# Kernel tuning notes

Measured on AMD Instinct MI355X. Metric: run time of the kernel, lower is better.

Reference implementation:

```python
import jax, jax.numpy as jnp
import numpy as np

N_NODES = 100000
N_EDGES = 1600000
IN_F = 64
HID_F = 64
HID_CH = 32
OUT_F = 16


def setup_inputs() -> dict:
    key = jax.random.key(0)
    ks = jax.random.split(key, 12)
    feat = jax.random.normal(ks[0], (N_NODES, IN_F), dtype=jnp.float32)
    edge_src = jax.random.randint(ks[1], (N_EDGES,), 0, N_NODES, dtype=jnp.int32)
    edge_dst = jax.random.randint(ks[2], (N_EDGES,), 0, N_NODES, dtype=jnp.int32)
    s = 1.414 / np.sqrt(IN_F)
    fc1_w = jax.random.normal(ks[3], (HID_F, IN_F), dtype=jnp.float32) * s
    fc1_b = jnp.zeros((HID_F,), dtype=jnp.float32)
    filt_w = jax.random.normal(ks[4], (HID_F, IN_F), dtype=jnp.float32) * s
    filt_b = jnp.zeros((HID_F,), dtype=jnp.float32)
    att_w1 = jax.random.normal(ks[5], (HID_F, HID_CH), dtype=jnp.float32) * (1.0 / np.sqrt(HID_F))
    att_b1 = jnp.zeros((HID_CH,), dtype=jnp.float32)
    att_w2 = jax.random.normal(ks[6], (HID_CH, 1), dtype=jnp.float32) * (1.0 / np.sqrt(HID_CH))
    fc2_w = jax.random.normal(ks[7], (OUT_F, HID_F), dtype=jnp.float32) * (1.414 / np.sqrt(HID_F))
    fc2_b = jnp.zeros((OUT_F,), dtype=jnp.float32)
    return {
        "feat": feat, "edge_src": edge_src, "edge_dst": edge_dst,
        "fc1_w": fc1_w, "fc1_b": fc1_b, "filt_w": filt_w, "filt_b": filt_b,
        "att_w1": att_w1, "att_b1": att_b1, "att_w2": att_w2,
        "fc2_w": fc2_w, "fc2_b": fc2_b,
    }


def _lp_filter(feat, edge_src, edge_dst, filt_w, filt_b):
    # Low-pass (GCN-style) filter: symmetric-normalized neighborhood aggregation
    # of the linearly transformed features.  x: [N, H]
    x = feat @ filt_w.T + filt_b
    ones = jnp.ones((edge_src.shape[0],), dtype=x.dtype)
    deg_out = jax.ops.segment_sum(ones, edge_src, num_segments=N_NODES)
    deg_in = jax.ops.segment_sum(ones, edge_dst, num_segments=N_NODES)
    inv_sqrt_out = jax.lax.rsqrt(jnp.maximum(deg_out, 1.0))
    inv_sqrt_in = jax.lax.rsqrt(jnp.maximum(deg_in, 1.0))
    # gather-transform-scatter: msg_e = x[src_e] * norm_e  ->  sum at dst
    coef = inv_sqrt_out[edge_src] * inv_sqrt_in[edge_dst]  # [E]
    msg = x[edge_src] * coef[:, None]                       # [E, H]
    return jax.ops.segment_sum(msg, edge_dst, num_segments=N_NODES)  # [N, H]


def _channel_attention(z, att_w1, att_b1, att_w2):
    # z: [N, C, H]; semantic (channel) attention a la HAN
    w = jnp.tanh(z @ att_w1 + att_b1) @ att_w2        # [N, C, 1]
    beta = jax.nn.softmax(w.mean(axis=0), axis=0)     # [C, 1]
    return (beta[None, :, :] * z).sum(axis=1)         # [N, H]


def reference(feat, edge_src, edge_dst, fc1_w, fc1_b, filt_w, filt_b,
              att_w1, att_b1, att_w2, fc2_w, fc2_b):
    h1 = jnp.tanh(feat @ fc1_w.T + fc1_b)                          # MLP branch [N, H]
    h2 = _lp_filter(feat, edge_src, edge_dst, filt_w, filt_b)      # graph branch [N, H]
    z = jnp.stack([h1, h2], axis=1)                                # [N, 2, H]
    fused = _channel_attention(z, att_w1, att_b1, att_w2)          # [N, H]
    return fused @ fc2_w.T + fc2_b                                 # [N, OUT_F]
```

## Files before the change

### kernel.cpp

```cpp
#include <hip/hip_runtime.h>
#include <math.h>

#define N_NODESC 100000
#define N_EDGESC 1600000
#define NBUCK 1563
#define BSLACK 1280
#define SCHUNK 4096
#define NSBLK 391

__device__ __forceinline__ float fast_tanh(float x) {
    float ax = fabsf(x);
    float e = __expf(-2.f * ax);
    float r = (1.f - e) * __builtin_amdgcn_rcpf(1.f + e);
    return copysignf(r, x);
}

__global__ void binit_kernel(int* __restrict__ bcur, int* __restrict__ sbcur) {
    int i = blockIdx.x * blockDim.x + threadIdx.x;
    if (i < NBUCK) { bcur[i] = i * BSLACK; sbcur[i] = i * BSLACK; }
}

__global__ __launch_bounds__(1024) void scatter_dual_kernel(
    const int* __restrict__ src, const int* __restrict__ dst,
    int* __restrict__ bcur, int* __restrict__ sbcur,
    unsigned* __restrict__ bedges, unsigned char* __restrict__ sbytes) {
    __shared__ int histd[NBUCK];
    __shared__ int hists[NBUCK];
    int tid = threadIdx.x;
    int e_beg = blockIdx.x * SCHUNK;
    int e_end = min(e_beg + SCHUNK, N_EDGESC);
    for (int i = tid; i < NBUCK; i += 1024) { histd[i] = 0; hists[i] = 0; }
    __syncthreads();

    int ss[4], dd[4];
    int cnt = 0;
    for (int i = e_beg + tid; i < e_end; i += 1024) {
        ss[cnt] = src[i];
        dd[cnt] = dst[i];
        cnt++;
    }
#pragma unroll
    for (int j = 0; j < 4; j++) {
        if (j < cnt) {
            atomicAdd(&histd[dd[j] >> 6], 1);
            atomicAdd(&hists[ss[j] >> 6], 1);
        }
    }
    __syncthreads();
    for (int i = tid; i < NBUCK; i += 1024) {
        int c = histd[i];
        if (c > 0) histd[i] = atomicAdd(&bcur[i], c);
        int c2 = hists[i];
        if (c2 > 0) hists[i] = atomicAdd(&sbcur[i], c2);
    }
    __syncthreads();
#pragma unroll
    for (int j = 0; j < 4; j++) {
        if (j < cnt) {
            int slot = atomicAdd(&histd[dd[j] >> 6], 1);
            bedges[slot] = (unsigned)ss[j] | ((unsigned)(dd[j] & 63) << 17);
            int slot2 = atomicAdd(&hists[ss[j] >> 6], 1);
            sbytes[slot2] = (unsigned char)(ss[j] & 63);
        }
    }
}

__global__ __launch_bounds__(256) void gemm_kernel(
    const float* __restrict__ feat,
    const float* __restrict__ w1, const float* __restrict__ b1,
    const float* __restrict__ w2, const float* __restrict__ b2,
    const int* __restrict__ sbcur, const unsigned char* __restrict__ sbytes,
    float* __restrict__ h1, float* __restrict__ xs) {
    __shared__ float sf[128 * 68];
    __shared__ int ldeg[128];
    int tid = threadIdx.x;
    int base = blockIdx.x * 128;
    if (tid < 128) ldeg[tid] = 0;
    for (int k = 0; k < 8; k++) {
        int fi = tid + k * 256;
        int node = fi >> 4, f4 = fi & 15;
        float4 v = make_float4(0.f, 0.f, 0.f, 0.f);
        if (base + node < N_NODESC)
            v = ((const float4*)feat)[(size_t)(base + node) * 16 + f4];
        float* d = &sf[node * 68 + f4 * 4];
        d[0] = v.x; d[1] = v.y; d[2] = v.z; d[3] = v.w;
    }
    __syncthreads();

#pragma unroll
    for (int h = 0; h < 2; h++) {
        int sb = blockIdx.x * 2 + h;
        if (sb < NBUCK) {
            int sbeg = sb * BSLACK;
            int sm = sbcur[sb] - sbeg;
            for (int i = tid; i < sm; i += 256)
                atomicAdd(&ldeg[h * 64 + (int)sbytes[sbeg + i]], 1);
        }
    }

    int lane = tid & 63;
    int og = __builtin_amdgcn_readfirstlane(tid >> 6);
    const float* wp1 = w1 + og * 16 * 64;
    const float* wp2 = w2 + og * 16 * 64;

    float a1[2][16], a2[2][16];
#pragma unroll
    for (int o = 0; o < 16; o++) {
        float bb1 = b1[og * 16 + o], bb2 = b2[og * 16 + o];
        a1[0][o] = bb1; a1[1][o] = bb1;
        a2[0][o] = bb2; a2[1][o] = bb2;
    }

    for (int fq = 0; fq < 16; fq++) {
        float4 fv0 = *(const float4*)&sf[lane * 68 + fq * 4];
        float4 fv1 = *(const float4*)&sf[(lane + 64) * 68 + fq * 4];
#pragma unroll
        for (int o = 0; o < 16; o++) {
            float4 wv1 = *(const float4*)&wp1[o * 64 + fq * 4];
            float4 wv2 = *(const float4*)&wp2[o * 64 + fq * 4];
            a1[0][o] += fv0.x * wv1.x + fv0.y * wv1.y + fv0.z * wv1.z + fv0.w * wv1.w;
            a1[1][o] += fv1.x * wv1.x + fv1.y * wv1.y + fv1.z * wv1.z + fv1.w * wv1.w;
            a2[0][o] += fv0.x * wv2.x + fv0.y * wv2.y + fv0.z * wv2.z + fv0.w * wv2.w;
            a2[1][o] += fv1.x * wv2.x + fv1.y * wv2.y + fv1.z * wv2.z + fv1.w * wv2.w;
        }
    }

    __syncthreads();

#pragma unroll
    for (int j = 0; j < 2; j++) {
        int g = base + lane + j * 64;
        if (g >= N_NODESC) continue;
        float is = rsqrtf(fmaxf((float)ldeg[j * 64 + lane], 1.f));
#pragma unroll
        for (int oq = 0; oq < 4; oq++) {
            float4 t, u;
            t.x = fast_tanh(a1[j][oq * 4 + 0]); t.y = fast_tanh(a1[j][oq * 4 + 1]);
            t.z = fast_tanh(a1[j][oq * 4 + 2]); t.w = fast_tanh(a1[j][oq * 4 + 3]);
            u.x = a2[j][oq * 4 + 0] * is;   u.y = a2[j][oq * 4 + 1] * is;
            u.z = a2[j][oq * 4 + 2] * is;   u.w = a2[j][oq * 4 + 3] * is;
            ((float4*)h1)[(size_t)g * 16 + og * 4 + oq] = t;
            ((float4*)xs)[(size_t)g * 16 + og * 4 + oq] = u;
        }
    }
}

__global__ __launch_bounds__(256) void agg4_kernel(const int* __restrict__ bcur,
                                                   const unsigned* __restrict__ bedges,
                                                   const float* __restrict__ xs,
                                                   float* __restrict__ h2) {
    __shared__ unsigned eraw[BSLACK];
    __shared__ unsigned eled[BSLACK];
    __shared__ int loff[65];
    __shared__ int lcnt[64];
    __shared__ int lcur[64];
    int tid = threadIdx.x, lane = tid & 63, wid = tid >> 6;
    int b = blockIdx.x;
    int beg = b * BSLACK;
    int m = bcur[b] - beg;

    if (tid < 64) lcnt[tid] = 0;
    __syncthreads();
    for (int i = tid; i < m; i += 256) {
        unsigned pk = bedges[beg + i];
        eraw[i] = pk;
        atomicAdd(&lcnt[pk >> 17], 1);
    }
    __syncthreads();
    if (wid == 0) {
        int c = lcnt[lane];
        int v = c;
#pragma unroll
        for (int off = 1; off < 64; off <<= 1) {
            int t = __shfl_up(v, off, 64);
            if (lane >= off) v += t;
        }
        loff[lane] = v - c;
        lcur[lane] = v - c;
        if (lane == 63) loff[64] = v;
    }
    __syncthreads();
    for (int i = tid; i < m; i += 256) {
        unsigned pk = eraw[i];
        int pos = atomicAdd(&lcur[pk >> 17], 1);
        eled[pos] = pk & 0x1FFFFu;
    }
    __syncthreads();

    int nbase = b * 64;
#pragma unroll 1
    for (int t = 0; t < 16; t++) {
        int nl = wid * 16 + t;
        int s0 = loff[nl], s1 = loff[nl + 1];
        float acc = 0.f;
        for (int k = s0; k < s1; k += 16) {
            int cnt = s1 - k; if (cnt > 16) cnt = 16;
            unsigned sv = eled[min(k + (lane & 15), s1 - 1)];
            float v[16];
#pragma unroll
            for (int j = 0; j < 16; j++) {
                if (j < cnt) {
                    int sj = __shfl((int)sv, j, 64);
                    v[j] = xs[(size_t)sj * 64 + lane];
                }
            }
#pragma unroll
            for (int j = 0; j < 16; j++)
                if (j < cnt) acc += v[j];
        }
        int g = nbase + nl;
        if (g < N_NODESC) {
            float isq = rsqrtf(fmaxf((float)(s1 - s0), 1.f));
            h2[(size_t)g * 64 + lane] = acc * isq;
        }
    }
}

__global__ __launch_bounds__(256) void att3_kernel(const float* __restrict__ h1,
                                                   const float* __restrict__ h2,
                                                   const float* __restrict__ aw1,
                                                   const float* __restrict__ ab1,
                                                   const float* __restrict__ aw2,
                                                   float* __restrict__ wsum) {
    __shared__ float sf[2][64 * 68];
    __shared__ float ssc[2][2][64];
    int tid = threadIdx.x, lane = tid & 63;
    int wid = __builtin_amdgcn_readfirstlane(tid >> 6);
    int br = wid >> 1, cg = wid & 1;
    int base = blockIdx.x * 64;

#pragma unroll
    for (int b = 0; b < 2; b++) {
        const float* H = b ? h2 : h1;
#pragma unroll
        for (int k = 0; k < 4; k++) {
            int fi = tid + k * 256;
            int node = fi >> 4, f4 = fi & 15;
            float4 v = make_float4(0.f, 0.f, 0.f, 0.f);
            if (base + node < N_NODESC)
                v = ((const float4*)H)[(size_t)(base + node) * 16 + f4];
            float* d = &sf[b][node * 68 + f4 * 4];
            d[0] = v.x; d[1] = v.y; d[2] = v.z; d[3] = v.w;
        }
    }
    __syncthreads();

    float acc[16];
#pragma unroll
    for (int c = 0; c < 16; c++) acc[c] = ab1[cg * 16 + c];
    const float* sfb = &sf[br][lane * 68];
    for (int fq = 0; fq < 16; fq++) {
        float4 hv = *(const float4*)&sfb[fq * 4];
#pragma unroll
        for (int k = 0; k < 4; k++) {
            float h = (k == 0) ? hv.x : (k == 1) ? hv.y : (k == 2) ? hv.z : hv.w;
            const float* wp = &aw1[(fq * 4 + k) * 32 + cg * 16];
#pragma unroll
            for (int cq = 0; cq < 4; cq++) {
                float4 wv = *(const float4*)&wp[cq * 4];
                acc[cq * 4 + 0] += h * wv.x; acc[cq * 4 + 1] += h * wv.y;
                acc[cq * 4 + 2] += h * wv.z; acc[cq * 4 + 3] += h * wv.w;
            }
        }
    }
    float s = 0.f;
#pragma unroll
    for (int c = 0; c < 16; c++) s += fast_tanh(acc[c]) * aw2[cg * 16 + c];
    ssc[br][cg][lane] = s;
    __syncthreads();

    if (tid < 128) {
        int b2 = tid >> 6, node = tid & 63;
        float v = ssc[b2][0][node] + ssc[b2][1][node];
        if (base + node >= N_NODESC) v = 0.f;
#pragma unroll
        for (int off = 32; off; off >>= 1) v += __shfl_down(v, off, 64);
        if (node == 0) atomicAdd(&wsum[b2], v);
    }
}

__global__ __launch_bounds__(256) void out_kernel(const float* __restrict__ h1,
                                                  const float* __restrict__ h2,
                                                  const float* __restrict__ wsum,
                                                  const float* __restrict__ w,
                                                  const float* __restrict__ b,
                                                  float* __restrict__ out) {
    __shared__ float sw[16 * 68];
    int tid = threadIdx.x;
    {
        int o = tid >> 4, f4 = tid & 15;
        float4 v = ((const float4*)w)[tid];
        float* d = &sw[o * 68 + f4 * 4];
        d[0] = v.x; d[1] = v.y; d[2] = v.z; d[3] = v.w;
    }
    __syncthreads();
    float w0 = wsum[0] * (1.f / (float)N_NODESC);
    float w1 = wsum[1] * (1.f / (float)N_NODESC);
    float mx = fmaxf(w0, w1);
    float e0 = __expf(w0 - mx), e1 = __expf(w1 - mx);
    float inv = 1.f / (e0 + e1);
    float b0 = e0 * inv, b1v = e1 * inv;

    int o = tid & 15, ln = tid >> 4;
    int node = blockIdx.x * 16 + ln;
    if (node >= N_NODESC) return;
    const float4* r1 = (const float4*)(h1 + (size_t)node * 64);
    const float4* r2 = (const float4*)(h2 + (size_t)node * 64);
    float acc = b[o];
    for (int fq = 0; fq < 16; fq++) {
        float4 x1 = r1[fq], x2 = r2[fq];
        float4 wv = *(const float4*)&sw[o * 68 + fq * 4];
        acc += (b0 * x1.x + b1v * x2.x) * wv.x + (b0 * x1.y + b1v * x2.y) * wv.y
             + (b0 * x1.z + b1v * x2.z) * wv.z + (b0 * x1.w + b1v * x2.w) * wv.w;
    }
    out[(size_t)node * 16 + o] = acc;
}

extern "C" void kernel_launch(void* const* d_in, const int* in_sizes, int n_in,
                              void* d_out, int out_size, void* d_ws, size_t ws_size,
                              hipStream_t stream) {
    (void)in_sizes; (void)n_in; (void)out_size; (void)ws_size;
    const float* feat = (const float*)d_in[0];
    const int*   esrc = (const int*)d_in[1];
    const int*   edst = (const int*)d_in[2];
    const float* fc1w = (const float*)d_in[3];
    const float* fc1b = (const float*)d_in[4];
    const float* fltw = (const float*)d_in[5];
    const float* fltb = (const float*)d_in[6];
    const float* aw1  = (const float*)d_in[7];
    const float* ab1  = (const float*)d_in[8];
    const float* aw2  = (const float*)d_in[9];
    const float* fc2w = (const float*)d_in[10];
    const float* fc2b = (const float*)d_in[11];
    float* out = (float*)d_out;

    char* ws = (char*)d_ws;
    size_t off = 0;
    auto alloc = [&](size_t bytes) {
        char* p = ws + off;
        off += (bytes + 255) & ~(size_t)255;
        return p;
    };
    float*         h1     = (float*)alloc((size_t)N_NODESC * 64 * 4);
    float*         xs     = (float*)alloc((size_t)N_NODESC * 64 * 4);
    float*         h2     = (float*)alloc((size_t)N_NODESC * 64 * 4);
    int*           bcur   = (int*)alloc((size_t)NBUCK * 4);
    int*           sbcur  = (int*)alloc((size_t)NBUCK * 4);
    unsigned*      bedges = (unsigned*)alloc((size_t)NBUCK * BSLACK * 4);
    unsigned char* sbytes = (unsigned char*)alloc((size_t)NBUCK * BSLACK);
    float*         wsum   = (float*)alloc(16 * 4);

    hipMemsetAsync(wsum, 0, 2 * 4, stream);

    binit_kernel<<<(NBUCK + 255) / 256, 256, 0, stream>>>(bcur, sbcur);
    scatter_dual_kernel<<<NSBLK, 1024, 0, stream>>>(esrc, edst, bcur, sbcur,
                                                    bedges, sbytes);
    gemm_kernel<<<(N_NODESC + 127) / 128, 256, 0, stream>>>(
        feat, fc1w, fc1b, fltw, fltb, sbcur, sbytes, h1, xs);
    agg4_kernel<<<NBUCK, 256, 0, stream>>>(bcur, bedges, xs, h2);
    att3_kernel<<<NBUCK, 256, 0, stream>>>(h1, h2, aw1, ab1, aw2, wsum);
    out_kernel<<<(N_NODESC + 15) / 16, 256, 0, stream>>>(h1, h2, wsum,
                                                         fc2w, fc2b, out);
}
```

Baseline: 310.6 us.

## Store scaled filter features in fp16 and gather two edges per wavefront

```diff
diff --git a/kernel.cpp b/kernel.cpp
--- a/kernel.cpp
+++ b/kernel.cpp
@@ -1,4 +1,5 @@
 #include <hip/hip_runtime.h>
+#include <hip/hip_fp16.h>
 #include <math.h>
 
 #define N_NODESC 100000
@@ -70,7 +71,7 @@
     const float* __restrict__ w1, const float* __restrict__ b1,
     const float* __restrict__ w2, const float* __restrict__ b2,
     const int* __restrict__ sbcur, const unsigned char* __restrict__ sbytes,
-    float* __restrict__ h1, float* __restrict__ xs) {
+    float* __restrict__ h1, __half* __restrict__ xs) {
     __shared__ float sf[128 * 68];
     __shared__ int ldeg[128];
     int tid = threadIdx.x;
@@ -134,20 +135,23 @@
         float is = rsqrtf(fmaxf((float)ldeg[j * 64 + lane], 1.f));
 #pragma unroll
         for (int oq = 0; oq < 4; oq++) {
-            float4 t, u;
+            float4 t;
             t.x = fast_tanh(a1[j][oq * 4 + 0]); t.y = fast_tanh(a1[j][oq * 4 + 1]);
             t.z = fast_tanh(a1[j][oq * 4 + 2]); t.w = fast_tanh(a1[j][oq * 4 + 3]);
-            u.x = a2[j][oq * 4 + 0] * is;   u.y = a2[j][oq * 4 + 1] * is;
-            u.z = a2[j][oq * 4 + 2] * is;   u.w = a2[j][oq * 4 + 3] * is;
             ((float4*)h1)[(size_t)g * 16 + og * 4 + oq] = t;
-            ((float4*)xs)[(size_t)g * 16 + og * 4 + oq] = u;
-        }
-    }
-}
-
-__global__ __launch_bounds__(256) void agg4_kernel(const int* __restrict__ bcur,
+            ushort4 us;
+            us.x = __half_as_ushort(__float2half_rn(a2[j][oq * 4 + 0] * is));
+            us.y = __half_as_ushort(__float2half_rn(a2[j][oq * 4 + 1] * is));
+            us.z = __half_as_ushort(__float2half_rn(a2[j][oq * 4 + 2] * is));
+            us.w = __half_as_ushort(__float2half_rn(a2[j][oq * 4 + 3] * is));
+            ((ushort4*)xs)[(size_t)g * 16 + og * 4 + oq] = us;
+        }
+    }
+}
+
+__global__ __launch_bounds__(256) void agg5_kernel(const int* __restrict__ bcur,
                                                    const unsigned* __restrict__ bedges,
-                                                   const float* __restrict__ xs,
+                                                   const __half* __restrict__ xs,
                                                    float* __restrict__ h2) {
     __shared__ unsigned eraw[BSLACK];
     __shared__ unsigned eled[BSLACK];
@@ -188,30 +192,44 @@
     __syncthreads();
 
     int nbase = b * 64;
+    int lo = lane & 31;
+    int hi = lane >> 5;
+    int voffb = lo * 4;
 #pragma unroll 1
     for (int t = 0; t < 16; t++) {
         int nl = wid * 16 + t;
         int s0 = loff[nl], s1 = loff[nl + 1];
-        float acc = 0.f;
-        for (int k = s0; k < s1; k += 16) {
-            int cnt = s1 - k; if (cnt > 16) cnt = 16;
-            unsigned sv = eled[min(k + (lane & 15), s1 - 1)];
-            float v[16];
+        float ax = 0.f, ay = 0.f;
+        for (int k = s0; k < s1; k += 32) {
+            int cnt = s1 - k; if (cnt > 32) cnt = 32;
+            int npair = (cnt + 1) >> 1;
+            unsigned sv = eled[min(k + lo, s1 - 1)];
+            float vx[16], vy[16];
 #pragma unroll
             for (int j = 0; j < 16; j++) {
-                if (j < cnt) {
-                    int sj = __shfl((int)sv, j, 64);
-                    v[j] = xs[(size_t)sj * 64 + lane];
+                if (j < npair) {
+                    int sjA = __shfl((int)sv, 2 * j, 64);
+                    int sjB = __shfl((int)sv, 2 * j + 1, 64);
+                    const char* basep = (const char*)(xs + (size_t)sjA * 64);
+                    int rowd = (sjB - sjA) * 128;
+                    int off = voffb + (hi ? rowd : 0);
+                    __half2 hv = *(const __half2*)(basep + off);
+                    float2 f = __half22float2(hv);
+                    float msk = (hi && (k + 2 * j + 1 >= s1)) ? 0.f : 1.f;
+                    vx[j] = f.x * msk; vy[j] = f.y * msk;
                 }
             }
 #pragma unroll
             for (int j = 0; j < 16; j++)
-                if (j < cnt) acc += v[j];
-        }
+                if (j < npair) { ax += vx[j]; ay += vy[j]; }
+        }
+        ax += __shfl_xor(ax, 32, 64);
+        ay += __shfl_xor(ay, 32, 64);
         int g = nbase + nl;
-        if (g < N_NODESC) {
+        if (g < N_NODESC && lane < 32) {
             float isq = rsqrtf(fmaxf((float)(s1 - s0), 1.f));
-            h2[(size_t)g * 64 + lane] = acc * isq;
+            float2 o = make_float2(ax * isq, ay * isq);
+            *(float2*)&h2[(size_t)g * 64 + lo * 2] = o;
         }
     }
 }
@@ -342,7 +360,7 @@
         return p;
     };
     float*         h1     = (float*)alloc((size_t)N_NODESC * 64 * 4);
-    float*         xs     = (float*)alloc((size_t)N_NODESC * 64 * 4);
+    __half*        xs     = (__half*)alloc((size_t)N_NODESC * 64 * 2);
     float*         h2     = (float*)alloc((size_t)N_NODESC * 64 * 4);
     int*           bcur   = (int*)alloc((size_t)NBUCK * 4);
     int*           sbcur  = (int*)alloc((size_t)NBUCK * 4);
@@ -357,7 +375,7 @@
                                                     bedges, sbytes);
     gemm_kernel<<<(N_NODESC + 127) / 128, 256, 0, stream>>>(
         feat, fc1w, fc1b, fltw, fltb, sbcur, sbytes, h1, xs);
-    agg4_kernel<<<NBUCK, 256, 0, stream>>>(bcur, bedges, xs, h2);
+    agg5_kernel<<<NBUCK, 256, 0, stream>>>(bcur, bedges, xs, h2);
     att3_kernel<<<NBUCK, 256, 0, stream>>>(h1, h2, aw1, ab1, aw2, wsum);
     out_kernel<<<(N_NODESC + 15) / 16, 256, 0, stream>>>(h1, h2, wsum,
                                                          fc2w, fc2b, out);
```

Measured after the change: 377.5 us. 21.5% more time.
